# Kernel tuning notes

Hardware: AMD Instinct MI355X
Metric: run time of the kernel (lower is better)

## Reference

```python
import jax, jax.numpy as jnp
import numpy as np

N_X, N_M, E, D_IN, D_OUT = 200000, 50000, 600000, 128, 128
BN_EPS = 1e-5


def setup_inputs() -> dict:
    key = jax.random.key(0)
    ks = jax.random.split(key, 12)
    s = 0.02
    x_metrical = jax.random.normal(ks[0], (N_M, D_IN), dtype=jnp.float32)
    x = jax.random.normal(ks[1], (N_X, D_IN), dtype=jnp.float32)
    src = jax.random.randint(ks[2], (E,), 0, N_X)   # indexes x (note nodes)
    dst = jax.random.randint(ks[3], (E,), 0, N_M)   # indexes x_metrical
    edge_index = jnp.stack([src, dst], axis=0)
    batch = jnp.zeros((N_M,), dtype=jnp.int64 if jax.config.jax_enable_x64 else jnp.int32)
    return {
        "x_metrical": x_metrical,
        "x": x,
        "edge_index": edge_index,
        "batch": batch,
        "W_neigh": jax.random.normal(ks[4], (D_IN, D_IN), dtype=jnp.float32) * s,
        "b_neigh": jnp.zeros((D_IN,), dtype=jnp.float32),
        "W_l": jax.random.normal(ks[5], (D_IN, D_IN), dtype=jnp.float32) * s,  # SAGEConv lin_l (neighbors)
        "b_l": jnp.zeros((D_IN,), dtype=jnp.float32),
        "W_r": jax.random.normal(ks[6], (D_IN, D_IN), dtype=jnp.float32) * s,  # SAGEConv lin_r (root, no bias)
        "W_out": jax.random.normal(ks[7], (D_OUT, 3 * D_IN), dtype=jnp.float32) * s,
        "b_out": jnp.zeros((D_OUT,), dtype=jnp.float32),
        "gamma": jnp.ones((D_OUT,), dtype=jnp.float32),
        "beta": jnp.zeros((D_OUT,), dtype=jnp.float32),
    }


def reference(x_metrical, x, edge_index, batch, W_neigh, b_neigh, W_l, b_l, W_r,
              W_out, b_out, gamma, beta):
    n_m = x_metrical.shape[0]
    n_x = x.shape[0]
    src, dst = edge_index[0], edge_index[1]

    # neigh linear on note features, scatter-add onto metrical nodes
    h_neigh = x @ W_neigh.T + b_neigh                          # [N_x, D]
    h_scatter = jax.ops.segment_sum(h_neigh[src], dst, num_segments=n_m)  # [N_m, D]

    # SAGEConv(aggr='add') over the chain seq_index (batch all-equal branch):
    # edge i -> i+1, so sum-aggregation = shift x_metrical down by one row.
    agg = jnp.concatenate(
        [jnp.zeros((1, x_metrical.shape[1]), dtype=x_metrical.dtype), x_metrical[:-1]],
        axis=0)
    h_seq = agg @ W_l.T + b_l + x_metrical @ W_r.T             # [N_m, D]

    # concat + output linear (activation = Identity)
    h = jnp.concatenate([h_scatter, x_metrical, h_seq], axis=1)  # [N_m, 3D]
    h = h @ W_out.T + b_out                                      # [N_m, D_out]

    # BatchNorm1d (training-mode batch stats, biased variance); dropout = identity (eval)
    mean = jnp.mean(h, axis=0)
    var = jnp.mean((h - mean) ** 2, axis=0)
    h = (h - mean) * jax.lax.rsqrt(var + BN_EPS) * gamma + beta

    # final scatter-add back onto note nodes
    out = jax.ops.segment_sum(h[dst], src, num_segments=n_x)     # [N_x, D_out]
    return out
```

## Files before the change

### kernel.cpp

```cpp
#include <hip/hip_runtime.h>

#define D_IN 128
#define BN_EPS 1e-5f
#define BIN_SHIFT 8
#define MAXBIN 1024

typedef __attribute__((ext_vector_type(8))) __bf16 bf16x8;
typedef __attribute__((ext_vector_type(8))) unsigned short ushort8;
typedef __attribute__((ext_vector_type(4))) float f32x4;
typedef unsigned short ushort_t;

__device__ inline ushort_t f2bf(float x) {
    union { float f; unsigned u; } c; c.f = x;
    unsigned r = (c.u + 0x7fffu + ((c.u >> 16) & 1u)) >> 16;
    return (ushort_t)r;
}
__device__ inline float bf2f(ushort_t x) {
    union { unsigned u; float f; } c; c.u = ((unsigned)x) << 16;
    return c.f;
}
__device__ inline float lof(unsigned v) {
    union { unsigned u; float f; } c; c.u = v << 16;
    return c.f;
}
__device__ inline float hif(unsigned v) {
    union { unsigned u; float f; } c; c.u = v & 0xffff0000u;
    return c.f;
}

__global__ void cvt2_k(const float* __restrict__ a, const float* __restrict__ b,
                       ushort_t* __restrict__ oa, ushort_t* __restrict__ ob,
                       int n8a, int n8b) {
    int i = blockIdx.x * blockDim.x + threadIdx.x;
    const float* in; ushort_t* out; int k;
    if (i < n8a) { in = a; out = oa; k = i; }
    else if (i < n8a + n8b) { in = b; out = ob; k = i - n8a; }
    else return;
    float4 f0 = ((const float4*)in)[k * 2];
    float4 f1 = ((const float4*)in)[k * 2 + 1];
    ushort8 o;
    o[0] = f2bf(f0.x); o[1] = f2bf(f0.y); o[2] = f2bf(f0.z); o[3] = f2bf(f0.w);
    o[4] = f2bf(f1.x); o[5] = f2bf(f1.y); o[6] = f2bf(f1.z); o[7] = f2bf(f1.w);
    ((ushort8*)out)[k] = o;
}

__global__ void combine_weights_k(const float* __restrict__ Wn, const float* __restrict__ bn,
                                  const float* __restrict__ Wl, const float* __restrict__ bl,
                                  const float* __restrict__ Wr, const float* __restrict__ Wo,
                                  const float* __restrict__ bo,
                                  ushort_t* __restrict__ Wb, float* __restrict__ c1,
                                  float* __restrict__ c0,
                                  int* __restrict__ binCnt) {
    int b = blockIdx.x;
    int j = threadIdx.x;
    if (b < 384) {
        int term = b >> 7;
        int k = b & 127;
        float acc = 0.f;
        if (term == 0) {
            for (int t = 0; t < 128; ++t) acc += Wo[j * 384 + t] * Wn[t * 128 + k];
        } else if (term == 1) {
            acc = Wo[j * 384 + 128 + k];
            for (int t = 0; t < 128; ++t) acc += Wo[j * 384 + 256 + t] * Wr[t * 128 + k];
        } else {
            for (int t = 0; t < 128; ++t) acc += Wo[j * 384 + 256 + t] * Wl[t * 128 + k];
        }
        Wb[term * 16384 + j * 128 + k] = f2bf(acc);
    } else if (b == 384) {
        float a1 = 0.f, a0 = bo[j];
        for (int t = 0; t < 128; ++t) {
            a1 += Wo[j * 384 + t] * bn[t];
            a0 += Wo[j * 384 + 256 + t] * bl[t];
        }
        c1[j] = a1;
        c0[j] = a0;
    } else {
        for (int i = j; i < MAXBIN; i += 128) binCnt[i] = 0;
    }
}


__global__ __launch_bounds__(256) void bin_hist_k(const int* __restrict__ src,
                                                  const int* __restrict__ dst,
                                                  int* __restrict__ binCnt,
                                                  int nE, int nM, int nBin) {
    __shared__ int h[MAXBIN];
    int t = threadIdx.x;
    for (int i = t; i < nBin; i += 256) h[i] = 0;
    __syncthreads();
    int total = 2 * nE;
    int per = (total + gridDim.x - 1) / gridDim.x;
    int lo = blockIdx.x * per, hi = min(lo + per, total);
    for (int i = lo + t; i < hi; i += 256) {
        int key = (i < nE) ? dst[i] : (nM + src[i - nE]);
        atomicAdd(&h[key >> BIN_SHIFT], 1);
    }
    __syncthreads();
    for (int i = t; i < nBin; i += 256) {
        int v = h[i];
        if (v) atomicAdd(&binCnt[i], v);
    }
}

__global__ __launch_bounds__(1024) void bin_scan_k(const int* __restrict__ binCnt,
                                                   int* __restrict__ binBase,
                                                   int* __restrict__ binCursor,
                                                   int* __restrict__ offs,
                                                   int nBin, int nTot, int total2E) {
    __shared__ int sc[1024];
    int t = threadIdx.x;
    int v = (t < nBin) ? binCnt[t] : 0;
    sc[t] = v;
    __syncthreads();
    for (int off = 1; off < 1024; off <<= 1) {
        int a = (t >= off) ? sc[t - off] : 0;
        __syncthreads();
        sc[t] += a;
        __syncthreads();
    }
    int excl = sc[t] - v;
    if (t <= nBin) binBase[t] = excl;
    if (t < nBin) binCursor[t] = excl;
    if (t == nBin) offs[nTot] = total2E;
}

__global__ __launch_bounds__(256) void bin_scatter_k(const int* __restrict__ src,
                                                     const int* __restrict__ dst,
                                                     int* __restrict__ binCursor,
                                                     unsigned* __restrict__ binned,
                                                     int nE, int nM, int nBin) {
    __shared__ int h[MAXBIN];
    __shared__ int base[MAXBIN];
    int t = threadIdx.x;
    for (int i = t; i < nBin; i += 256) h[i] = 0;
    __syncthreads();
    int total = 2 * nE;
    int per = (total + gridDim.x - 1) / gridDim.x;
    int lo = blockIdx.x * per, hi = min(lo + per, total);
    for (int i = lo + t; i < hi; i += 256) {
        int key = (i < nE) ? dst[i] : (nM + src[i - nE]);
        atomicAdd(&h[key >> BIN_SHIFT], 1);
    }
    __syncthreads();
    for (int i = t; i < nBin; i += 256) {
        int c = h[i];
        base[i] = c ? atomicAdd(&binCursor[i], c) : 0;
        h[i] = 0;
    }
    __syncthreads();
    for (int i = lo + t; i < hi; i += 256) {
        int key, val;
        if (i < nE) { key = dst[i]; val = src[i]; }
        else        { key = nM + src[i - nE]; val = dst[i - nE]; }
        int b = key >> BIN_SHIFT;
        int p = base[b] + atomicAdd(&h[b], 1);
        binned[p] = ((unsigned)(key & ((1 << BIN_SHIFT) - 1)) << 20) | (unsigned)val;
    }
}

__global__ __launch_bounds__(256) void bucket_sort_k(const unsigned* __restrict__ binned,
                                                     const int* __restrict__ binBase,
                                                     int* __restrict__ offs,
                                                     int* __restrict__ list, int nTot) {
    __shared__ int hist[256];
    __shared__ int sc[256];
    __shared__ int cur[256];
    int b = blockIdx.x;
    int base = binBase[b], end = binBase[b + 1];
    int n = end - base;
    int t = threadIdx.x;
    hist[t] = 0;
    __syncthreads();
    for (int i = t; i < n; i += 256) atomicAdd(&hist[binned[base + i] >> 20], 1);
    __syncthreads();
    int v = hist[t];
    sc[t] = v;
    __syncthreads();
    for (int off = 1; off < 256; off <<= 1) {
        int a = (t >= off) ? sc[t - off] : 0;
        __syncthreads();
        sc[t] += a;
        __syncthreads();
    }
    int excl = sc[t] - v;
    int bucket = (b << BIN_SHIFT) + t;
    if (bucket < nTot) offs[bucket] = base + excl;
    cur[t] = excl;
    __syncthreads();
    for (int i = t; i < n; i += 256) {
        unsigned p = binned[base + i];
        int lb = p >> 20;
        int pos = atomicAdd(&cur[lb], 1);
        list[base + pos] = (int)(p & 0xFFFFFu);
    }
}


__global__ __launch_bounds__(256) void gather_xs_k(const uint2* __restrict__ x4,
                                                   const int* __restrict__ offs,
                                                   const int* __restrict__ list,
                                                   uint2* __restrict__ XS4, int nM) {
    int m = blockIdx.x * 8 + (threadIdx.x >> 5);
    if (m >= nM) return;
    int l = threadIdx.x & 31;
    int s = offs[m], e = offs[m + 1];
    float a0 = 0.f, a1 = 0.f, a2 = 0.f, a3 = 0.f;
    for (int s0 = s; s0 < e; s0 += 32) {
        int cnt = min(e - s0, 32);
        int r = (l < cnt) ? list[s0 + l] : 0;
        for (int i0 = 0; i0 < cnt; i0 += 8) {
            uint2 v[8];
#pragma unroll
            for (int j = 0; j < 8; ++j) {
                int idx = i0 + j;
                int cl = idx < cnt ? idx : cnt - 1;
                int rr = __shfl(r, cl, 32);
                v[j] = x4[(size_t)rr * 32 + l];
            }
#pragma unroll
            for (int j = 0; j < 8; ++j) {
                if (i0 + j < cnt) {
                    a0 += lof(v[j].x); a1 += hif(v[j].x);
                    a2 += lof(v[j].y); a3 += hif(v[j].y);
                }
            }
        }
    }
    uint2 o;
    o.x = (unsigned)f2bf(a0) | ((unsigned)f2bf(a1) << 16);
    o.y = (unsigned)f2bf(a2) | ((unsigned)f2bf(a3) << 16);
    XS4[(size_t)m * 32 + l] = o;
}

__global__ __launch_bounds__(256) void gemm_h_k(const ushort_t* __restrict__ XSb,
                                                const ushort_t* __restrict__ XMb,
                                                const ushort_t* __restrict__ Wb,
                                                const float* __restrict__ c1,
                                                const float* __restrict__ c0,
                                                const int* __restrict__ off,
                                                ushort_t* __restrict__ Hb,
                                                float* __restrict__ partS,
                                                float* __restrict__ partQ, int nM) {
    __shared__ float lds_s[4][128];
    __shared__ float lds_q[4][128];
    int wave = threadIdx.x >> 6, lane = threadIdx.x & 63;
    int m0 = blockIdx.x * 64 + wave * 16;
    int rl = lane & 15, kg = lane >> 4;
    f32x4 acc[8];
#pragma unroll
    for (int jt = 0; jt < 8; ++jt) acc[jt] = (f32x4){0.f, 0.f, 0.f, 0.f};
    int arow = m0 + rl;
    bool wave_live = (m0 < nM);
    if (wave_live) {
#pragma unroll
        for (int term = 0; term < 3; ++term) {
            const ushort_t* xp = (term == 0) ? XSb : XMb;
            int r2 = (term == 2) ? (arow - 1) : arow;
            bool valid = (r2 >= 0) && (arow < nM);
            const ushort_t* rp = xp + (size_t)r2 * D_IN + kg * 8;
            const ushort_t* wbase = Wb + term * 16384 + rl * 128 + kg * 8;
            bf16x8 a[4];
#pragma unroll
            for (int kc = 0; kc < 4; ++kc) {
                if (valid) {
                    a[kc] = *reinterpret_cast<const bf16x8*>(rp + kc * 32);
                } else {
#pragma unroll
                    for (int i = 0; i < 8; ++i) a[kc][i] = (__bf16)0.f;
                }
            }
#pragma unroll
            for (int kc = 0; kc < 4; ++kc) {
                bf16x8 bfr[8];
#pragma unroll
                for (int jt = 0; jt < 8; ++jt)
                    bfr[jt] = *reinterpret_cast<const bf16x8*>(wbase + jt * 2048 + kc * 32);
#pragma unroll
                for (int jt = 0; jt < 8; ++jt)
                    acc[jt] = __builtin_amdgcn_mfma_f32_16x16x32_bf16(a[kc], bfr[jt], acc[jt], 0, 0, 0);
            }
        }
    }
    float ssum[8], sq[8];
#pragma unroll
    for (int jt = 0; jt < 8; ++jt) { ssum[jt] = 0.f; sq[jt] = 0.f; }
    if (wave_live) {
        float cc1[8], cc0[8];
#pragma unroll
        for (int jt = 0; jt < 8; ++jt) { cc1[jt] = c1[jt * 16 + rl]; cc0[jt] = c0[jt * 16 + rl]; }
#pragma unroll
        for (int r = 0; r < 4; ++r) {
            int rowd = m0 + kg * 4 + r;
            if (rowd < nM) {
                float degv = (float)(off[rowd + 1] - off[rowd]);
                ushort_t* hp = Hb + (size_t)rowd * D_IN;
#pragma unroll
                for (int jt = 0; jt < 8; ++jt) {
                    float hv = acc[jt][r] + degv * cc1[jt] + cc0[jt];
                    hp[jt * 16 + rl] = f2bf(hv);
                    ssum[jt] += hv;
                    sq[jt] += hv * hv;
                }
            }
        }
    }
#pragma unroll
    for (int jt = 0; jt < 8; ++jt) {
        ssum[jt] += __shfl_xor(ssum[jt], 16, 64);
        ssum[jt] += __shfl_xor(ssum[jt], 32, 64);
        sq[jt]   += __shfl_xor(sq[jt], 16, 64);
        sq[jt]   += __shfl_xor(sq[jt], 32, 64);
    }
    if (lane < 16) {
#pragma unroll
        for (int jt = 0; jt < 8; ++jt) {
            lds_s[wave][jt * 16 + rl] = ssum[jt];
            lds_q[wave][jt * 16 + rl] = sq[jt];
        }
    }
    __syncthreads();
    if (threadIdx.x < 128) {
        int col = threadIdx.x;
        float s = lds_s[0][col] + lds_s[1][col] + lds_s[2][col] + lds_s[3][col];
        float q = lds_q[0][col] + lds_q[1][col] + lds_q[2][col] + lds_q[3][col];
        partS[(size_t)blockIdx.x * 128 + col] = s;
        partQ[(size_t)blockIdx.x * 128 + col] = q;
    }
}

__global__ __launch_bounds__(1024) void bn_reduce_k(const float* __restrict__ partS,
                                                    const float* __restrict__ partQ,
                                                    float* __restrict__ bnsum,
                                                    float* __restrict__ bnsq, int nB) {
    __shared__ float ls[8][128], lq[8][128];
    int col = threadIdx.x & 127, seg = threadIdx.x >> 7;
    float s = 0.f, q = 0.f;
    for (int b = seg; b < nB; b += 8) {
        s += partS[(size_t)b * 128 + col];
        q += partQ[(size_t)b * 128 + col];
    }
    ls[seg][col] = s;
    lq[seg][col] = q;
    __syncthreads();
    if (threadIdx.x < 128) {
        float S = 0.f, Q = 0.f;
#pragma unroll
        for (int i = 0; i < 8; ++i) { S += ls[i][col]; Q += lq[i][col]; }
        bnsum[col] = S;
        bnsq[col] = Q;
    }
}

__global__ __launch_bounds__(256) void gather_out_k(const uint2* __restrict__ H4,
                                                    const int* __restrict__ offs2,
                                                    const int* __restrict__ list,
                                                    const float* __restrict__ bnsum,
                                                    const float* __restrict__ bnsq,
                                                    const float* __restrict__ gamma,
                                                    const float* __restrict__ beta,
                                                    float4* __restrict__ out4,
                                                    int nX, int nM) {
    int n = blockIdx.x * 8 + (threadIdx.x >> 5);
    if (n >= nX) return;
    int l = threadIdx.x & 31;
    int s = offs2[n], e = offs2[n + 1];
    float a0 = 0.f, a1 = 0.f, a2 = 0.f, a3 = 0.f;
    for (int s0 = s; s0 < e; s0 += 32) {
        int cnt = min(e - s0, 32);
        int r = (l < cnt) ? list[s0 + l] : 0;
        for (int i0 = 0; i0 < cnt; i0 += 4) {
            uint2 v[4];
#pragma unroll
            for (int j = 0; j < 4; ++j) {
                int idx = i0 + j;
                int cl = idx < cnt ? idx : cnt - 1;
                int rr = __shfl(r, cl, 32);
                v[j] = H4[(size_t)rr * 32 + l];
            }
#pragma unroll
            for (int j = 0; j < 4; ++j) {
                if (i0 + j < cnt) {
                    a0 += lof(v[j].x); a1 += hif(v[j].x);
                    a2 += lof(v[j].y); a3 += hif(v[j].y);
                }
            }
        }
    }
    float4 s1 = ((const float4*)bnsum)[l];
    float4 s2 = ((const float4*)bnsq)[l];
    float4 g  = ((const float4*)gamma)[l];
    float4 be = ((const float4*)beta)[l];
    float inv = 1.0f / (float)nM;
    float cnt = (float)(e - s);
    float4 o;
    {
        float mean = s1.x * inv, var = s2.x * inv - mean * mean;
        float sc = g.x * rsqrtf(var + BN_EPS);
        o.x = sc * a0 + cnt * (be.x - mean * sc);
    }
    {
        float mean = s1.y * inv, var = s2.y * inv - mean * mean;
        float sc = g.y * rsqrtf(var + BN_EPS);
        o.y = sc * a1 + cnt * (be.y - mean * sc);
    }
    {
        float mean = s1.z * inv, var = s2.z * inv - mean * mean;
        float sc = g.z * rsqrtf(var + BN_EPS);
        o.z = sc * a2 + cnt * (be.z - mean * sc);
    }
    {
        float mean = s1.w * inv, var = s2.w * inv - mean * mean;
        float sc = g.w * rsqrtf(var + BN_EPS);
        o.w = sc * a3 + cnt * (be.w - mean * sc);
    }
    out4[(size_t)n * 32 + l] = o;
}

extern "C" void kernel_launch(void* const* d_in, const int* in_sizes, int n_in,
                              void* d_out, int out_size, void* d_ws, size_t ws_size,
                              hipStream_t stream) {
    const float* x_metrical = (const float*)d_in[0];
    const float* x          = (const float*)d_in[1];
    const int*   edge       = (const int*)d_in[2];
    const float* Wn    = (const float*)d_in[4];
    const float* bn    = (const float*)d_in[5];
    const float* Wl    = (const float*)d_in[6];
    const float* bl    = (const float*)d_in[7];
    const float* Wr    = (const float*)d_in[8];
    const float* Wo    = (const float*)d_in[9];
    const float* bo    = (const float*)d_in[10];
    const float* gamma = (const float*)d_in[11];
    const float* beta  = (const float*)d_in[12];
    float* out = (float*)d_out;

    int nM = in_sizes[0] / D_IN;
    int nX = in_sizes[1] / D_IN;
    int nE = in_sizes[2] / 2;
    int nTot = nM + nX;
    int nBin = (nTot + 255) >> BIN_SHIFT;
    int nBlkGemm = (nM + 63) / 64;
    const int* src = edge;
    const int* dst = edge + nE;

    char* ws = (char*)d_ws;
    size_t o = 0;
    auto alloc = [&](size_t bytes) -> void* {
        void* p = ws + o;
        o = (o + bytes + 255) & ~(size_t)255;
        return p;
    };
    ushort_t* Wb        = (ushort_t*)alloc((size_t)3 * 128 * 128 * 2);
    float*    c1        = (float*)alloc(512);
    float*    c0        = (float*)alloc(512);
    float*    bnsum     = (float*)alloc(512);
    float*    bnsq      = (float*)alloc(512);
    int*      binCnt    = (int*)alloc(4096);
    int*      binBase   = (int*)alloc(4104);
    int*      binCursor = (int*)alloc(4096);
    float*    partS     = (float*)alloc((size_t)nBlkGemm * 128 * 4);
    float*    partQ     = (float*)alloc((size_t)nBlkGemm * 128 * 4);
    int*      offs      = (int*)alloc(((size_t)nTot + 1) * 4);
    int*      list      = (int*)alloc((size_t)2 * nE * 4);
    size_t unionSz = (size_t)2 * nE * 4;
    size_t xsSz = (size_t)nM * D_IN * 2;
    char* uregion = (char*)alloc(unionSz > xsSz ? unionSz : xsSz);
    unsigned* binned = (unsigned*)uregion;
    ushort_t* XSb    = (ushort_t*)uregion;
    ushort_t* xmb    = (ushort_t*)alloc((size_t)nM * D_IN * 2);
    ushort_t* xb     = (ushort_t*)alloc((size_t)nX * D_IN * 2);
    ushort_t* Hb     = xb;

    combine_weights_k<<<386, 128, 0, stream>>>(Wn, bn, Wl, bl, Wr, Wo, bo, Wb, c1, c0,
                                               binCnt);
    {
        int n8x = nX * D_IN / 8, n8m = nM * D_IN / 8;
        cvt2_k<<<(n8x + n8m + 255) / 256, 256, 0, stream>>>(x, x_metrical, xb, xmb, n8x, n8m);
    }
    bin_hist_k<<<256, 256, 0, stream>>>(src, dst, binCnt, nE, nM, nBin);
    bin_scan_k<<<1, 1024, 0, stream>>>(binCnt, binBase, binCursor, offs, nBin, nTot, 2 * nE);
    bin_scatter_k<<<256, 256, 0, stream>>>(src, dst, binCursor, binned, nE, nM, nBin);
    bucket_sort_k<<<nBin, 256, 0, stream>>>(binned, binBase, offs, list, nTot);
    gather_xs_k<<<(nM + 7) / 8, 256, 0, stream>>>((const uint2*)xb, offs, list,
                                                  (uint2*)XSb, nM);
    gemm_h_k<<<nBlkGemm, 256, 0, stream>>>(XSb, xmb, Wb, c1, c0, offs, Hb,
                                           partS, partQ, nM);
    bn_reduce_k<<<1, 1024, 0, stream>>>(partS, partQ, bnsum, bnsq, nBlkGemm);
    gather_out_k<<<(nX + 7) / 8, 256, 0, stream>>>((const uint2*)Hb, offs + nM, list,
                                                   bnsum, bnsq, gamma, beta,
                                                   (float4*)out, nX, nM);
}
```

Baseline: 245.8 us.

## Gather fp32 x directly, drop bulk bf16 conversion, fuse x_metrical convert

Drops the pass that converted all of x to bf16. gather_xs_k now reads the fp32 rows directly with float4 loads. The smaller x_metrical conversion moves into extra blocks of combine_weights_k, which removes one launch, and H gets its own buffer. The final output store becomes nontemporal. This avoids reading and writing the 200k-row x just to convert it, but doubles the bytes of each random gather from x.

```diff
diff --git a/kernel.cpp b/kernel.cpp
--- a/kernel.cpp
+++ b/kernel.cpp
@@ -26,22 +26,6 @@
 __device__ inline float hif(unsigned v) {
     union { unsigned u; float f; } c; c.u = v & 0xffff0000u;
     return c.f;
-}
-
-__global__ void cvt2_k(const float* __restrict__ a, const float* __restrict__ b,
-                       ushort_t* __restrict__ oa, ushort_t* __restrict__ ob,
-                       int n8a, int n8b) {
-    int i = blockIdx.x * blockDim.x + threadIdx.x;
-    const float* in; ushort_t* out; int k;
-    if (i < n8a) { in = a; out = oa; k = i; }
-    else if (i < n8a + n8b) { in = b; out = ob; k = i - n8a; }
-    else return;
-    float4 f0 = ((const float4*)in)[k * 2];
-    float4 f1 = ((const float4*)in)[k * 2 + 1];
-    ushort8 o;
-    o[0] = f2bf(f0.x); o[1] = f2bf(f0.y); o[2] = f2bf(f0.z); o[3] = f2bf(f0.w);
-    o[4] = f2bf(f1.x); o[5] = f2bf(f1.y); o[6] = f2bf(f1.z); o[7] = f2bf(f1.w);
-    ((ushort8*)out)[k] = o;
 }
 
 __global__ void combine_weights_k(const float* __restrict__ Wn, const float* __restrict__ bn,
@@ -50,7 +34,9 @@
                                   const float* __restrict__ bo,
                                   ushort_t* __restrict__ Wb, float* __restrict__ c1,
                                   float* __restrict__ c0,
-                                  int* __restrict__ binCnt) {
+                                  int* __restrict__ binCnt,
+                                  const float* __restrict__ xm, ushort_t* __restrict__ xmb,
+                                  int n8m) {
     int b = blockIdx.x;
     int j = threadIdx.x;
     if (b < 384) {
@@ -74,8 +60,18 @@
         }
         c1[j] = a1;
         c0[j] = a0;
+    } else if (b == 385) {
+        for (int i = j; i < MAXBIN; i += 128) binCnt[i] = 0;
     } else {
-        for (int i = j; i < MAXBIN; i += 128) binCnt[i] = 0;
+        int i = (b - 386) * 128 + j;
+        if (i < n8m) {
+            float4 f0 = ((const float4*)xm)[i * 2];
+            float4 f1 = ((const float4*)xm)[i * 2 + 1];
+            ushort8 o;
+            o[0] = f2bf(f0.x); o[1] = f2bf(f0.y); o[2] = f2bf(f0.z); o[3] = f2bf(f0.w);
+            o[4] = f2bf(f1.x); o[5] = f2bf(f1.y); o[6] = f2bf(f1.z); o[7] = f2bf(f1.w);
+            ((ushort8*)xmb)[i] = o;
+        }
     }
 }
 
@@ -196,7 +192,7 @@
 }
 
 
-__global__ __launch_bounds__(256) void gather_xs_k(const uint2* __restrict__ x4,
+__global__ __launch_bounds__(256) void gather_xs_k(const float4* __restrict__ x4,
                                                    const int* __restrict__ offs,
                                                    const int* __restrict__ list,
                                                    uint2* __restrict__ XS4, int nM) {
@@ -209,7 +205,7 @@
         int cnt = min(e - s0, 32);
         int r = (l < cnt) ? list[s0 + l] : 0;
         for (int i0 = 0; i0 < cnt; i0 += 8) {
-            uint2 v[8];
+            float4 v[8];
 #pragma unroll
             for (int j = 0; j < 8; ++j) {
                 int idx = i0 + j;
@@ -220,8 +216,7 @@
 #pragma unroll
             for (int j = 0; j < 8; ++j) {
                 if (i0 + j < cnt) {
-                    a0 += lof(v[j].x); a1 += hif(v[j].x);
-                    a2 += lof(v[j].y); a3 += hif(v[j].y);
+                    a0 += v[j].x; a1 += v[j].y; a2 += v[j].z; a3 += v[j].w;
                 }
             }
         }
@@ -358,7 +353,7 @@
                                                     const float* __restrict__ bnsq,
                                                     const float* __restrict__ gamma,
                                                     const float* __restrict__ beta,
-                                                    float4* __restrict__ out4,
+                                                    float* __restrict__ out,
                                                     int nX, int nM) {
     int n = blockIdx.x * 8 + (threadIdx.x >> 5);
     if (n >= nX) return;
@@ -392,7 +387,7 @@
     float4 be = ((const float4*)beta)[l];
     float inv = 1.0f / (float)nM;
     float cnt = (float)(e - s);
-    float4 o;
+    f32x4 o;
     {
         float mean = s1.x * inv, var = s2.x * inv - mean * mean;
         float sc = g.x * rsqrtf(var + BN_EPS);
@@ -413,7 +408,7 @@
         float sc = g.w * rsqrtf(var + BN_EPS);
         o.w = sc * a3 + cnt * (be.w - mean * sc);
     }
-    out4[(size_t)n * 32 + l] = o;
+    __builtin_nontemporal_store(o, (f32x4*)(out + (size_t)n * 128 + l * 4));
 }
 
 extern "C" void kernel_launch(void* const* d_in, const int* in_sizes, int n_in,
@@ -467,25 +462,22 @@
     unsigned* binned = (unsigned*)uregion;
     ushort_t* XSb    = (ushort_t*)uregion;
     ushort_t* xmb    = (ushort_t*)alloc((size_t)nM * D_IN * 2);
-    ushort_t* xb     = (ushort_t*)alloc((size_t)nX * D_IN * 2);
-    ushort_t* Hb     = xb;
-
-    combine_weights_k<<<386, 128, 0, stream>>>(Wn, bn, Wl, bl, Wr, Wo, bo, Wb, c1, c0,
-                                               binCnt);
-    {
-        int n8x = nX * D_IN / 8, n8m = nM * D_IN / 8;
-        cvt2_k<<<(n8x + n8m + 255) / 256, 256, 0, stream>>>(x, x_metrical, xb, xmb, n8x, n8m);
-    }
+    ushort_t* Hb     = (ushort_t*)alloc((size_t)nM * D_IN * 2);
+
+    int n8m = nM * D_IN / 8;
+    int nBlkComb = 386 + (n8m + 127) / 128;
+    combine_weights_k<<<nBlkComb, 128, 0, stream>>>(Wn, bn, Wl, bl, Wr, Wo, bo, Wb, c1, c0,
+                                                    binCnt, x_metrical, xmb, n8m);
     bin_hist_k<<<256, 256, 0, stream>>>(src, dst, binCnt, nE, nM, nBin);
     bin_scan_k<<<1, 1024, 0, stream>>>(binCnt, binBase, binCursor, offs, nBin, nTot, 2 * nE);
     bin_scatter_k<<<256, 256, 0, stream>>>(src, dst, binCursor, binned, nE, nM, nBin);
     bucket_sort_k<<<nBin, 256, 0, stream>>>(binned, binBase, offs, list, nTot);
-    gather_xs_k<<<(nM + 7) / 8, 256, 0, stream>>>((const uint2*)xb, offs, list,
+    gather_xs_k<<<(nM + 7) / 8, 256, 0, stream>>>((const float4*)x, offs, list,
                                                   (uint2*)XSb, nM);
     gemm_h_k<<<nBlkGemm, 256, 0, stream>>>(XSb, xmb, Wb, c1, c0, offs, Hb,
                                            partS, partQ, nM);
     bn_reduce_k<<<1, 1024, 0, stream>>>(partS, partQ, bnsum, bnsq, nBlkGemm);
     gather_out_k<<<(nX + 7) / 8, 256, 0, stream>>>((const uint2*)Hb, offs + nM, list,
                                                    bnsum, bnsq, gamma, beta,
-                                                   (float4*)out, nX, nM);
-}
+                                                   out, nX, nM);
+}
```

New measurement: 232.8 us. 5.3% less time.
